# Optimization experiments

Hardware: AMD Instinct MI355X
Metric: run time of the kernel (lower is better)

Reference implementation:

```python
import jax, jax.numpy as jnp
import numpy as np

N = 100000   # nodes
E = 1600000  # edges (avg degree 16)
F_IN = 128   # num_features
H = 128      # num_hidden
C = 40       # num_classes


def setup_inputs() -> dict:
    key = jax.random.key(0)
    ks = jax.random.split(key, 8)
    w = lambda k, sh: jax.random.normal(k, sh, dtype=jnp.float32) * 0.05
    return {
        "x": jax.random.normal(ks[0], (N, F_IN), dtype=jnp.float32),
        "edge_index": jax.random.randint(ks[1], (2, E), 0, N),
        "W_rel1": w(ks[2], (F_IN, H)),
        "b_rel1": jnp.zeros((H,), jnp.float32),
        "W_root1": w(ks[3], (F_IN, H)),
        "W_rel2": w(ks[4], (H, H)),
        "b_rel2": jnp.zeros((H,), jnp.float32),
        "W_root2": w(ks[5], (H, H)),
        "W_lin": w(ks[6], (2 * H, C)),
        "b_lin": jnp.zeros((C,), jnp.float32),
    }


def _graph_conv(x, src, dst, W_rel, b_rel, W_root, n):
    # PyG GraphConv: sum_{j in N(i)} x_j -> lin_rel, plus lin_root(x_i)
    agg = jax.ops.segment_sum(x[src], dst, num_segments=n)  # [N, d_in]
    return agg @ W_rel + b_rel + x @ W_root


def reference(x, edge_index, W_rel1, b_rel1, W_root1, W_rel2, b_rel2, W_root2, W_lin, b_lin):
    src, dst = edge_index[0], edge_index[1]
    n = x.shape[0]
    # dropout is identity at inference (training=False)
    x1 = jax.nn.relu(_graph_conv(x, src, dst, W_rel1, b_rel1, W_root1, n))
    x2 = jax.nn.relu(_graph_conv(x1, src, dst, W_rel2, b_rel2, W_root2, n))
    h = jnp.concatenate([x1, x2], axis=-1)  # [N, 2H]
    return jax.nn.log_softmax(h @ W_lin + b_lin, axis=-1)
```

## Files before the change

### kernel.cpp

```cpp
#include <hip/hip_runtime.h>
#include <hip/hip_bf16.h>

typedef __attribute__((ext_vector_type(8))) short bf16x8;
typedef __attribute__((ext_vector_type(4))) float f32x4;

#define EPB 4096
#define BUCKET_BITS 10
#define BUCKET_SIZE 1024

static __device__ __forceinline__ unsigned short f2bf(float f) {
    union { float f; unsigned u; } v; v.f = f;
    unsigned r = v.u + 0x7FFF + ((v.u >> 16) & 1);
    return (unsigned short)(r >> 16);
}
static __device__ __forceinline__ float asf(unsigned u) {
    union { unsigned u; float f; } v; v.u = u;
    return v.f;
}

__global__ __launch_bounds__(256) void prep(const float* __restrict__ Wrel1,
                                            const float* __restrict__ Wroot1,
                                            const float* __restrict__ Wrel2,
                                            const float* __restrict__ Wroot2,
                                            const float* __restrict__ Wlin,
                                            const int* __restrict__ dst,
                                            unsigned short* __restrict__ bsw1,
                                            unsigned short* __restrict__ bsw2,
                                            unsigned short* __restrict__ bswL,
                                            int* __restrict__ hist,
                                            int E, int nblk, int nbuck) {
    __shared__ int h[128];
    int blk = blockIdx.x, t = threadIdx.x;
    if (blk < 256) {
        const float* Wrel  = (blk < 128) ? Wrel1 : Wrel2;
        const float* Wroot = (blk < 128) ? Wroot1 : Wroot2;
        unsigned short* bsw = (blk < 128) ? bsw1 : bsw2;
        int idx = (blk & 127) * 256 + t;
        int j = idx & 7, L = (idx >> 3) & 63, ct = (idx >> 9) & 15, kt = idx >> 13;
        int k = kt * 32 + ((L >> 4) * 8) + j;
        int c = ct * 16 + (L & 15);
        float v = (c < 128) ? Wrel[k * 128 + c] : Wroot[k * 128 + (c - 128)];
        bsw[idx] = f2bf(v);
    } else if (blk < 304) {
        int idx = (blk - 256) * 256 + t;
        int tt = idx;
        int j = tt & 7; tt >>= 3;
        int L = tt & 63; tt >>= 6;
        int ct = tt % 3;
        int kt = tt / 3;
        int k = kt * 32 + ((L >> 4) * 8) + j;
        int c = ct * 16 + (L & 15);
        float v = (c < 40) ? Wlin[k * 40 + c] : 0.f;
        bswL[idx] = f2bf(v);
    } else {
        int hb = blk - 304;
        if (t < nbuck) h[t] = 0;
        __syncthreads();
        int e0 = hb * EPB;
#pragma unroll
        for (int it = 0; it < EPB / 256; it++) {
            int e = e0 + it * 256 + t;
            if (e < E) atomicAdd(&h[dst[e] >> BUCKET_BITS], 1);
        }
        __syncthreads();
        if (t < nbuck) hist[t * nblk + hb] = h[t];
    }
}

__global__ __launch_bounds__(256) void scan_all(int* __restrict__ hist,
                                                int* __restrict__ bucketBase,
                                                int nblk, int nbuck) {
    __shared__ int tot[128];
    __shared__ int s[256];
    int b = blockIdx.x, t = threadIdx.x;
    if (t < 128) tot[t] = 0;
    __syncthreads();
    int len = nbuck * nblk;
    for (int i = t; i < len; i += 256) atomicAdd(&tot[i / nblk], hist[i]);
    __syncthreads();
    if (t < 128) s[t] = tot[t];
    __syncthreads();
#pragma unroll
    for (int o = 1; o < 128; o <<= 1) {
        int x = (t < 128 && t >= o) ? s[t - o] : 0;
        __syncthreads();
        if (t < 128) s[t] += x;
        __syncthreads();
    }
    int base_b = s[b] - tot[b];
    int tot_b = tot[b];
    if (t == 0) {
        bucketBase[b] = base_b;
        if (b == nbuck - 1) bucketBase[nbuck] = base_b + tot_b;
    }
    __syncthreads();
    int carryv = base_b;
    for (int start = 0; start < nblk; start += 256) {
        int i = start + t;
        int v = (i < nblk) ? hist[b * nblk + i] : 0;
        s[t] = v; __syncthreads();
#pragma unroll
        for (int o = 1; o < 256; o <<= 1) {
            int x = (t >= o) ? s[t - o] : 0;
            __syncthreads();
            s[t] += x; __syncthreads();
        }
        int excl = s[t] - v + carryv;
        if (i < nblk) hist[b * nblk + i] = excl;
        carryv += s[255];
        __syncthreads();
    }
}

__global__ __launch_bounds__(256) void edge_part(const int* __restrict__ src,
                                                 const int* __restrict__ dst,
                                                 const int* __restrict__ hist,
                                                 int* __restrict__ part,
                                                 int E, int nblk, int nbuck) {
    __shared__ int hcnt[128];
    __shared__ int lstart[128];
    __shared__ int cur[128];
    __shared__ int gbase[128];
    __shared__ int ssc[128];
    __shared__ int sdst[EPB];
    __shared__ int ssrc[EPB];
    int t = threadIdx.x, blk = blockIdx.x;
    int e0 = blk * EPB;
    int cnt = E - e0; if (cnt > EPB) cnt = EPB;
    if (t < nbuck) { hcnt[t] = 0; gbase[t] = hist[t * nblk + blk]; }
    __syncthreads();
    int myd[EPB / 256], mys[EPB / 256];
#pragma unroll
    for (int it = 0; it < EPB / 256; it++) {
        int i = it * 256 + t;
        if (i < cnt) {
            myd[it] = dst[e0 + i];
            mys[it] = src[e0 + i];
            atomicAdd(&hcnt[myd[it] >> BUCKET_BITS], 1);
        }
    }
    __syncthreads();
    if (t < 128) ssc[t] = (t < nbuck) ? hcnt[t] : 0;
    __syncthreads();
#pragma unroll
    for (int o = 1; o < 128; o <<= 1) {
        int x = 0;
        if (t < 128 && t >= o) x = ssc[t - o];
        __syncthreads();
        if (t < 128) ssc[t] += x;
        __syncthreads();
    }
    if (t < nbuck) { lstart[t] = ssc[t] - hcnt[t]; cur[t] = 0; }
    __syncthreads();
#pragma unroll
    for (int it = 0; it < EPB / 256; it++) {
        int i = it * 256 + t;
        if (i < cnt) {
            int b = myd[it] >> BUCKET_BITS;
            int p = lstart[b] + atomicAdd(&cur[b], 1);
            sdst[p] = myd[it];
            ssrc[p] = mys[it];
        }
    }
    __syncthreads();
    for (int i = t; i < cnt; i += 256) {
        int d = sdst[i], s = ssrc[i];
        int b = d >> BUCKET_BITS;
        part[gbase[b] + (i - lstart[b])] = ((d & (BUCKET_SIZE - 1)) << 17) | s;
    }
}

__global__ __launch_bounds__(256) void csrfin_gemm1(const int* __restrict__ part,
                                                    const int* __restrict__ bucketBase,
                                                    int* __restrict__ off_,
                                                    int* __restrict__ deg_,
                                                    int* __restrict__ csr_src,
                                                    const float* __restrict__ x,
                                                    const unsigned short* __restrict__ Bsw,
                                                    const float* __restrict__ bias,
                                                    unsigned short* __restrict__ xr,
                                                    unsigned short* __restrict__ accbf,
                                                    int N, int nbuck) {
    __shared__ int cur[BUCKET_SIZE];
    __shared__ int h[BUCKET_SIZE];
    __shared__ int tsum[256];
    int t = threadIdx.x;
    if (blockIdx.x < (unsigned)nbuck) {
        int b = blockIdx.x;
        int lo = bucketBase[b], hi = bucketBase[b + 1];
        int n0 = b * BUCKET_SIZE;
        for (int i = t; i < BUCKET_SIZE; i += 256) h[i] = 0;
        __syncthreads();
        for (int i = lo + t; i < hi; i += 256) atomicAdd(&h[part[i] >> 17], 1);
        __syncthreads();
        int a0 = h[4 * t], a1 = h[4 * t + 1], a2 = h[4 * t + 2], a3 = h[4 * t + 3];
        int ts = a0 + a1 + a2 + a3;
        tsum[t] = ts;
        __syncthreads();
#pragma unroll
        for (int o = 1; o < 256; o <<= 1) {
            int xx = (t >= o) ? tsum[t - o] : 0;
            __syncthreads();
            tsum[t] += xx;
            __syncthreads();
        }
        int st0 = tsum[t] - ts;
        int st1 = st0 + a0, st2 = st1 + a1, st3 = st2 + a2;
        cur[4 * t] = st0; cur[4 * t + 1] = st1; cur[4 * t + 2] = st2; cur[4 * t + 3] = st3;
        int node = n0 + 4 * t;
        if (node < N)     { off_[node] = lo + st0;     deg_[node] = a0; }
        if (node + 1 < N) { off_[node + 1] = lo + st1; deg_[node + 1] = a1; }
        if (node + 2 < N) { off_[node + 2] = lo + st2; deg_[node + 2] = a2; }
        if (node + 3 < N) { off_[node + 3] = lo + st3; deg_[node + 3] = a3; }
        __syncthreads();
        for (int i = lo + t; i < hi; i += 256) {
            int rec = part[i];
            int p = atomicAdd(&cur[rec >> 17], 1);
            csr_src[lo + p] = rec & 0x1FFFF;
        }
    } else {
        int wid = (blockIdx.x - nbuck) * 4 + (t >> 6);
        int L = t & 63;
        int r0 = wid * 16;
        if (r0 >= N) return;
        int arow = r0 + (L & 15);
        const bf16x8* Bptr = ((const bf16x8*)Bsw) + L;
        f32x4 acc[16];
#pragma unroll
        for (int i = 0; i < 16; i++) acc[i] = (f32x4){0.f, 0.f, 0.f, 0.f};
#pragma unroll
        for (int kt = 0; kt < 4; kt++) {
            const float* Arow = x + (size_t)arow * 128 + ((L >> 4) * 8) + kt * 32;
            float4 a0 = *(const float4*)Arow;
            float4 a1 = *(const float4*)(Arow + 4);
            bf16x8 a;
            a[0] = (short)f2bf(a0.x); a[1] = (short)f2bf(a0.y);
            a[2] = (short)f2bf(a0.z); a[3] = (short)f2bf(a0.w);
            a[4] = (short)f2bf(a1.x); a[5] = (short)f2bf(a1.y);
            a[6] = (short)f2bf(a1.z); a[7] = (short)f2bf(a1.w);
#pragma unroll
            for (int ct = 0; ct < 16; ct++) {
                bf16x8 b = Bptr[(kt * 16 + ct) * 64];
                acc[ct] = __builtin_amdgcn_mfma_f32_16x16x32_bf16(a, b, acc[ct], 0, 0, 0);
            }
        }
        int rbase = r0 + (L >> 4) * 4;
        int cl = L & 15;
#pragma unroll
        for (int ct = 0; ct < 16; ct++) {
            int col = ct * 16 + cl;
#pragma unroll
            for (int r = 0; r < 4; r++) {
                int row = rbase + r;
                float v = acc[ct][r];
                if (col < 128)
                    xr[(size_t)row * 128 + col] = f2bf(v);
                else
                    accbf[(size_t)row * 128 + (col - 128)] = f2bf(v + bias[col - 128]);
            }
        }
    }
}

__global__ __launch_bounds__(256) void gemm_layer2(const unsigned short* __restrict__ Abf,
                                                   const unsigned short* __restrict__ Bsw,
                                                   const float* __restrict__ bias,
                                                   unsigned short* __restrict__ xr,
                                                   unsigned short* __restrict__ accbf, int N) {
    int wid = blockIdx.x * 4 + (threadIdx.x >> 6);
    int L = threadIdx.x & 63;
    int r0 = wid * 16;
    if (r0 >= N) return;
    int arow = r0 + (L & 15);
    const bf16x8* Bptr = ((const bf16x8*)Bsw) + L;
    f32x4 acc[16];
#pragma unroll
    for (int i = 0; i < 16; i++) acc[i] = (f32x4){0.f, 0.f, 0.f, 0.f};
#pragma unroll
    for (int kt = 0; kt < 4; kt++) {
        bf16x8 a = *((const bf16x8*)(Abf + (size_t)arow * 128 + ((L >> 4) * 8) + kt * 32));
#pragma unroll
        for (int ct = 0; ct < 16; ct++) {
            bf16x8 b = Bptr[(kt * 16 + ct) * 64];
            acc[ct] = __builtin_amdgcn_mfma_f32_16x16x32_bf16(a, b, acc[ct], 0, 0, 0);
        }
    }
    int rbase = r0 + (L >> 4) * 4;
    int cl = L & 15;
#pragma unroll
    for (int ct = 0; ct < 16; ct++) {
        int col = ct * 16 + cl;
#pragma unroll
        for (int r = 0; r < 4; r++) {
            int row = rbase + r;
            float v = acc[ct][r];
            if (col < 128)
                xr[(size_t)row * 128 + col] = f2bf(v);
            else
                accbf[(size_t)row * 128 + (col - 128)] = f2bf(v + bias[col - 128]);
        }
    }
}

__global__ __launch_bounds__(256) void agg_relu_cvt(const unsigned short* __restrict__ xr,
                                                    const unsigned short* __restrict__ accbf,
                                                    const int* __restrict__ off_,
                                                    const int* __restrict__ deg,
                                                    const int* __restrict__ csr_src,
                                                    unsigned short* __restrict__ out, int N) {
    int node = blockIdx.x * 4 + (threadIdx.x >> 6);
    if (node >= N) return;
    int L = threadIdx.x & 63;
    int g = L >> 4;
    int f = L & 15;
    int o = off_[node];
    int d = deg[node];
    uint4 arow = (uint4){0, 0, 0, 0};
    if (g == 0) arow = *(const uint4*)(accbf + (size_t)node * 128 + f * 8);

    float lo0 = 0.f, lo1 = 0.f, lo2 = 0.f, lo3 = 0.f;
    float hi0 = 0.f, hi1 = 0.f, hi2 = 0.f, hi3 = 0.f;

    for (int k = 0; k < d; k += 64) {
        int chunk = (d - k < 64) ? (d - k) : 64;
        int id = (L < chunk) ? csr_src[o + k + L] : 0;
        int full = chunk & ~3;
#pragma unroll 4
        for (int j = 0; j < full; j += 4) {
            int s = __shfl(id, j + g, 64);
            uint4 p = *(const uint4*)(xr + (size_t)s * 128 + f * 8);
            lo0 += asf(p.x << 16); hi0 += asf(p.x & 0xFFFF0000u);
            lo1 += asf(p.y << 16); hi1 += asf(p.y & 0xFFFF0000u);
            lo2 += asf(p.z << 16); hi2 += asf(p.z & 0xFFFF0000u);
            lo3 += asf(p.w << 16); hi3 += asf(p.w & 0xFFFF0000u);
        }
        if (full < chunk) {
            int sl = full + g;
            int s = __shfl(id, (sl < chunk) ? sl : 0, 64);
            if (sl < chunk) {
                uint4 p = *(const uint4*)(xr + (size_t)s * 128 + f * 8);
                lo0 += asf(p.x << 16); hi0 += asf(p.x & 0xFFFF0000u);
                lo1 += asf(p.y << 16); hi1 += asf(p.y & 0xFFFF0000u);
                lo2 += asf(p.z << 16); hi2 += asf(p.z & 0xFFFF0000u);
                lo3 += asf(p.w << 16); hi3 += asf(p.w & 0xFFFF0000u);
            }
        }
    }
    lo0 += __shfl_xor(lo0, 16, 64); hi0 += __shfl_xor(hi0, 16, 64);
    lo1 += __shfl_xor(lo1, 16, 64); hi1 += __shfl_xor(hi1, 16, 64);
    lo2 += __shfl_xor(lo2, 16, 64); hi2 += __shfl_xor(hi2, 16, 64);
    lo3 += __shfl_xor(lo3, 16, 64); hi3 += __shfl_xor(hi3, 16, 64);
    lo0 += __shfl_xor(lo0, 32, 64); hi0 += __shfl_xor(hi0, 32, 64);
    lo1 += __shfl_xor(lo1, 32, 64); hi1 += __shfl_xor(hi1, 32, 64);
    lo2 += __shfl_xor(lo2, 32, 64); hi2 += __shfl_xor(hi2, 32, 64);
    lo3 += __shfl_xor(lo3, 32, 64); hi3 += __shfl_xor(hi3, 32, 64);

    if (g == 0) {
        uint4 wv;
        wv.x = ((unsigned)f2bf(fmaxf(asf(arow.x & 0xFFFF0000u) + hi0, 0.f)) << 16)
             | f2bf(fmaxf(asf(arow.x << 16) + lo0, 0.f));
        wv.y = ((unsigned)f2bf(fmaxf(asf(arow.y & 0xFFFF0000u) + hi1, 0.f)) << 16)
             | f2bf(fmaxf(asf(arow.y << 16) + lo1, 0.f));
        wv.z = ((unsigned)f2bf(fmaxf(asf(arow.z & 0xFFFF0000u) + hi2, 0.f)) << 16)
             | f2bf(fmaxf(asf(arow.z << 16) + lo2, 0.f));
        wv.w = ((unsigned)f2bf(fmaxf(asf(arow.w & 0xFFFF0000u) + hi3, 0.f)) << 16)
             | f2bf(fmaxf(asf(arow.w << 16) + lo3, 0.f));
        *(uint4*)(out + (size_t)node * 128 + f * 8) = wv;
    }
}

__global__ __launch_bounds__(256) void gemm_final_ls(const unsigned short* __restrict__ x1bf,
                                                     const unsigned short* __restrict__ x2bf,
                                                     const unsigned short* __restrict__ Bsw,
                                                     const float* __restrict__ blin,
                                                     float* __restrict__ out, int N) {
    int wid = blockIdx.x * 4 + (threadIdx.x >> 6);
    int L = threadIdx.x & 63;
    int r0 = wid * 16;
    if (r0 >= N) return;
    int arow = r0 + (L & 15);
    f32x4 acc[3];
#pragma unroll
    for (int i = 0; i < 3; i++) acc[i] = (f32x4){0.f, 0.f, 0.f, 0.f};
#pragma unroll
    for (int kt = 0; kt < 8; kt++) {
        const unsigned short* Ab = (kt < 4) ? x1bf : x2bf;
        int kk = (kt & 3) * 32 + ((L >> 4) * 8);
        bf16x8 a = *((const bf16x8*)(Ab + (size_t)arow * 128 + kk));
#pragma unroll
        for (int ct = 0; ct < 3; ct++) {
            bf16x8 b = ((const bf16x8*)Bsw)[(kt * 3 + ct) * 64 + L];
            acc[ct] = __builtin_amdgcn_mfma_f32_16x16x32_bf16(a, b, acc[ct], 0, 0, 0);
        }
    }
    int rbase = r0 + (L >> 4) * 4;
    int cl = L & 15;
    float b0 = blin[cl], b1 = blin[16 + cl];
    float b2 = (cl < 8) ? blin[32 + cl] : 0.f;
#pragma unroll
    for (int r = 0; r < 4; r++) {
        int row = rbase + r;
        float v0 = acc[0][r] + b0;
        float v1 = acc[1][r] + b1;
        float v2 = (cl < 8) ? (acc[2][r] + b2) : -__builtin_inff();
        float m = fmaxf(fmaxf(v0, v1), v2);
#pragma unroll
        for (int off = 8; off >= 1; off >>= 1) m = fmaxf(m, __shfl_xor(m, off, 64));
        float e = __expf(v0 - m) + __expf(v1 - m) + ((cl < 8) ? __expf(v2 - m) : 0.f);
#pragma unroll
        for (int off = 8; off >= 1; off >>= 1) e += __shfl_xor(e, off, 64);
        float ls = m + __logf(e);
        float* op = out + (size_t)row * 40;
        op[cl] = v0 - ls;
        op[16 + cl] = v1 - ls;
        if (cl < 8) op[32 + cl] = v2 - ls;
    }
}

extern "C" void kernel_launch(void* const* d_in, const int* in_sizes, int n_in,
                              void* d_out, int out_size, void* d_ws, size_t ws_size,
                              hipStream_t stream) {
    const float* x      = (const float*)d_in[0];
    const int*   edge   = (const int*)d_in[1];
    const float* Wrel1  = (const float*)d_in[2];
    const float* brel1  = (const float*)d_in[3];
    const float* Wroot1 = (const float*)d_in[4];
    const float* Wrel2  = (const float*)d_in[5];
    const float* brel2  = (const float*)d_in[6];
    const float* Wroot2 = (const float*)d_in[7];
    const float* Wlin   = (const float*)d_in[8];
    const float* blin   = (const float*)d_in[9];

    const int N = in_sizes[0] / 128;
    const int E = in_sizes[1] / 2;
    const int* src = edge;
    const int* dst = edge + E;

    const int nblk  = (E + EPB - 1) / EPB;
    const int nbuck = (N + BUCKET_SIZE - 1) / BUCKET_SIZE;

    char* ws = (char*)d_ws;
    size_t off = 0;
    auto alloc = [&](size_t bytes) -> void* {
        void* p = ws + off;
        off += (bytes + 255) & ~(size_t)255;
        return p;
    };
    unsigned short* x1bf = (unsigned short*)alloc((size_t)N * 128 * 2);
    unsigned short* x2bf = (unsigned short*)alloc((size_t)N * 128 * 2);
    unsigned short* xr   = (unsigned short*)alloc((size_t)N * 128 * 2);
    unsigned short* accbf= (unsigned short*)alloc((size_t)N * 128 * 2);
    unsigned short* bsw1 = (unsigned short*)alloc(32768 * 2);
    unsigned short* bsw2 = (unsigned short*)alloc(32768 * 2);
    unsigned short* bswL = (unsigned short*)alloc(12288 * 2);
    int* hist       = (int*)alloc((size_t)nbuck * nblk * 4);
    int* bucketBase = (int*)alloc((size_t)(nbuck + 1) * 4);
    int* part       = (int*)alloc((size_t)E * 4);
    int* csr_src    = (int*)alloc((size_t)E * 4);
    int* off_       = (int*)alloc((size_t)N * 4);
    int* deg_       = (int*)alloc((size_t)N * 4);

    const int rowTiles = (N + 15) / 16;
    const int gemmBlocks = (rowTiles + 3) / 4;
    const int nodeBlocks = (N + 3) / 4;

    prep<<<304 + nblk, 256, 0, stream>>>(Wrel1, Wroot1, Wrel2, Wroot2, Wlin, dst,
                                         bsw1, bsw2, bswL, hist, E, nblk, nbuck);
    scan_all<<<nbuck, 256, 0, stream>>>(hist, bucketBase, nblk, nbuck);
    edge_part<<<nblk, 256, 0, stream>>>(src, dst, hist, part, E, nblk, nbuck);
    csrfin_gemm1<<<nbuck + gemmBlocks, 256, 0, stream>>>(part, bucketBase, off_, deg_, csr_src,
                                                         x, bsw1, brel1, xr, accbf, N, nbuck);
    agg_relu_cvt<<<nodeBlocks, 256, 0, stream>>>(xr, accbf, off_, deg_, csr_src, x1bf, N);
    gemm_layer2<<<gemmBlocks, 256, 0, stream>>>(x1bf, bsw2, brel2, xr, accbf, N);
    agg_relu_cvt<<<nodeBlocks, 256, 0, stream>>>(xr, accbf, off_, deg_, csr_src, x2bf, N);
    gemm_final_ls<<<gemmBlocks, 256, 0, stream>>>(x1bf, x2bf, bswL, blin, (float*)d_out, N);
}
```

Measured before the change: 383.1 us.

## Use finer node buckets, split bucket scan into three kernels, simplify gather loop

Bucket size drops from 1024 to 256 nodes, so the number of buckets rises from about 98 to about 391. That gives the CSR-finalize phase four times as many blocks and one node per thread. The single scan_all kernel, which made every block redundantly atomically total the whole histogram, is replaced by three kernels: per-bucket totals, one scan over buckets, and a per-bucket block scan. The aggregation loop now has each lane read its neighbor index directly from csr_src instead of loading a 64-entry chunk and broadcasting it with shuffles. In exchange there are two more kernel launches, a larger histogram, and more shared-memory arrays in edge_part.

```diff
diff --git a/kernel.cpp b/kernel.cpp
--- a/kernel.cpp
+++ b/kernel.cpp
@@ -5,8 +5,9 @@
 typedef __attribute__((ext_vector_type(4))) float f32x4;
 
 #define EPB 4096
-#define BUCKET_BITS 10
-#define BUCKET_SIZE 1024
+#define BUCKET_BITS 8
+#define BUCKET_SIZE 256
+#define MAXBUCK 512
 
 static __device__ __forceinline__ unsigned short f2bf(float f) {
     union { float f; unsigned u; } v; v.f = f;
@@ -29,7 +30,7 @@
                                             unsigned short* __restrict__ bswL,
                                             int* __restrict__ hist,
                                             int E, int nblk, int nbuck) {
-    __shared__ int h[128];
+    __shared__ int h[MAXBUCK];
     int blk = blockIdx.x, t = threadIdx.x;
     if (blk < 256) {
         const float* Wrel  = (blk < 128) ? Wrel1 : Wrel2;
@@ -54,7 +55,7 @@
         bswL[idx] = f2bf(v);
     } else {
         int hb = blk - 304;
-        if (t < nbuck) h[t] = 0;
+        for (int i = t; i < MAXBUCK; i += 256) h[i] = 0;
         __syncthreads();
         int e0 = hb * EPB;
 #pragma unroll
@@ -63,38 +64,49 @@
             if (e < E) atomicAdd(&h[dst[e] >> BUCKET_BITS], 1);
         }
         __syncthreads();
-        if (t < nbuck) hist[t * nblk + hb] = h[t];
-    }
-}
-
-__global__ __launch_bounds__(256) void scan_all(int* __restrict__ hist,
-                                                int* __restrict__ bucketBase,
-                                                int nblk, int nbuck) {
-    __shared__ int tot[128];
+        for (int i = t; i < nbuck; i += 256) hist[i * nblk + hb] = h[i];
+    }
+}
+
+__global__ __launch_bounds__(256) void bucket_total(const int* __restrict__ hist,
+                                                    int* __restrict__ total, int nblk) {
     __shared__ int s[256];
     int b = blockIdx.x, t = threadIdx.x;
-    if (t < 128) tot[t] = 0;
-    __syncthreads();
-    int len = nbuck * nblk;
-    for (int i = t; i < len; i += 256) atomicAdd(&tot[i / nblk], hist[i]);
-    __syncthreads();
-    if (t < 128) s[t] = tot[t];
-    __syncthreads();
-#pragma unroll
-    for (int o = 1; o < 128; o <<= 1) {
-        int x = (t < 128 && t >= o) ? s[t - o] : 0;
-        __syncthreads();
-        if (t < 128) s[t] += x;
-        __syncthreads();
-    }
-    int base_b = s[b] - tot[b];
-    int tot_b = tot[b];
-    if (t == 0) {
-        bucketBase[b] = base_b;
-        if (b == nbuck - 1) bucketBase[nbuck] = base_b + tot_b;
-    }
-    __syncthreads();
-    int carryv = base_b;
+    int v = 0;
+    for (int i = t; i < nblk; i += 256) v += hist[b * nblk + i];
+    s[t] = v; __syncthreads();
+#pragma unroll
+    for (int o = 128; o >= 1; o >>= 1) {
+        if (t < o) s[t] += s[t + o];
+        __syncthreads();
+    }
+    if (t == 0) total[b] = s[0];
+}
+
+__global__ __launch_bounds__(256) void bucket_scan(const int* __restrict__ total,
+                                                   int* __restrict__ base, int nbuck) {
+    __shared__ int s[256];
+    int t = threadIdx.x;
+    int e0 = (2 * t < nbuck) ? total[2 * t] : 0;
+    int e1 = (2 * t + 1 < nbuck) ? total[2 * t + 1] : 0;
+    int ps = e0 + e1;
+    s[t] = ps; __syncthreads();
+#pragma unroll
+    for (int o = 1; o < 256; o <<= 1) {
+        int x = (t >= o) ? s[t - o] : 0;
+        __syncthreads();
+        s[t] += x; __syncthreads();
+    }
+    int pbase = s[t] - ps;
+    if (2 * t <= nbuck) base[2 * t] = pbase;
+    if (2 * t + 1 <= nbuck) base[2 * t + 1] = pbase + e0;
+}
+
+__global__ __launch_bounds__(256) void block_scan(int* __restrict__ hist,
+                                                  const int* __restrict__ base, int nblk) {
+    __shared__ int s[256];
+    int b = blockIdx.x, t = threadIdx.x;
+    int carryv = base[b];
     for (int start = 0; start < nblk; start += 256) {
         int i = start + t;
         int v = (i < nblk) ? hist[b * nblk + i] : 0;
@@ -117,17 +129,18 @@
                                                  const int* __restrict__ hist,
                                                  int* __restrict__ part,
                                                  int E, int nblk, int nbuck) {
-    __shared__ int hcnt[128];
-    __shared__ int lstart[128];
-    __shared__ int cur[128];
-    __shared__ int gbase[128];
-    __shared__ int ssc[128];
+    __shared__ int hcnt[MAXBUCK];
+    __shared__ int lstart[MAXBUCK];
+    __shared__ int cur[MAXBUCK];
+    __shared__ int gbase[MAXBUCK];
+    __shared__ int s2[256];
     __shared__ int sdst[EPB];
     __shared__ int ssrc[EPB];
     int t = threadIdx.x, blk = blockIdx.x;
     int e0 = blk * EPB;
     int cnt = E - e0; if (cnt > EPB) cnt = EPB;
-    if (t < nbuck) { hcnt[t] = 0; gbase[t] = hist[t * nblk + blk]; }
+    for (int i = t; i < MAXBUCK; i += 256) hcnt[i] = 0;
+    for (int i = t; i < nbuck; i += 256) gbase[i] = hist[i * nblk + blk];
     __syncthreads();
     int myd[EPB / 256], mys[EPB / 256];
 #pragma unroll
@@ -140,17 +153,18 @@
         }
     }
     __syncthreads();
-    if (t < 128) ssc[t] = (t < nbuck) ? hcnt[t] : 0;
-    __syncthreads();
-#pragma unroll
-    for (int o = 1; o < 128; o <<= 1) {
-        int x = 0;
-        if (t < 128 && t >= o) x = ssc[t - o];
-        __syncthreads();
-        if (t < 128) ssc[t] += x;
-        __syncthreads();
-    }
-    if (t < nbuck) { lstart[t] = ssc[t] - hcnt[t]; cur[t] = 0; }
+    int p0 = hcnt[2 * t], p1 = hcnt[2 * t + 1];
+    int ps = p0 + p1;
+    s2[t] = ps; __syncthreads();
+#pragma unroll
+    for (int o = 1; o < 256; o <<= 1) {
+        int x = (t >= o) ? s2[t - o] : 0;
+        __syncthreads();
+        s2[t] += x; __syncthreads();
+    }
+    int pbase = s2[t] - ps;
+    lstart[2 * t] = pbase; lstart[2 * t + 1] = pbase + p0;
+    cur[2 * t] = 0; cur[2 * t + 1] = 0;
     __syncthreads();
 #pragma unroll
     for (int it = 0; it < EPB / 256; it++) {
@@ -189,13 +203,12 @@
         int b = blockIdx.x;
         int lo = bucketBase[b], hi = bucketBase[b + 1];
         int n0 = b * BUCKET_SIZE;
-        for (int i = t; i < BUCKET_SIZE; i += 256) h[i] = 0;
+        h[t] = 0;
         __syncthreads();
         for (int i = lo + t; i < hi; i += 256) atomicAdd(&h[part[i] >> 17], 1);
         __syncthreads();
-        int a0 = h[4 * t], a1 = h[4 * t + 1], a2 = h[4 * t + 2], a3 = h[4 * t + 3];
-        int ts = a0 + a1 + a2 + a3;
-        tsum[t] = ts;
+        int hv = h[t];
+        tsum[t] = hv;
         __syncthreads();
 #pragma unroll
         for (int o = 1; o < 256; o <<= 1) {
@@ -204,14 +217,10 @@
             tsum[t] += xx;
             __syncthreads();
         }
-        int st0 = tsum[t] - ts;
-        int st1 = st0 + a0, st2 = st1 + a1, st3 = st2 + a2;
-        cur[4 * t] = st0; cur[4 * t + 1] = st1; cur[4 * t + 2] = st2; cur[4 * t + 3] = st3;
-        int node = n0 + 4 * t;
-        if (node < N)     { off_[node] = lo + st0;     deg_[node] = a0; }
-        if (node + 1 < N) { off_[node + 1] = lo + st1; deg_[node + 1] = a1; }
-        if (node + 2 < N) { off_[node + 2] = lo + st2; deg_[node + 2] = a2; }
-        if (node + 3 < N) { off_[node + 3] = lo + st3; deg_[node + 3] = a3; }
+        int st = tsum[t] - hv;
+        cur[t] = st;
+        int node = n0 + t;
+        if (node < N) { off_[node] = lo + st; deg_[node] = hv; }
         __syncthreads();
         for (int i = lo + t; i < hi; i += 256) {
             int rec = part[i];
@@ -318,33 +327,29 @@
     uint4 arow = (uint4){0, 0, 0, 0};
     if (g == 0) arow = *(const uint4*)(accbf + (size_t)node * 128 + f * 8);
 
+    const int* ip = csr_src + o + g;
+    const unsigned short* xrf = xr + f * 8;
+
     float lo0 = 0.f, lo1 = 0.f, lo2 = 0.f, lo3 = 0.f;
     float hi0 = 0.f, hi1 = 0.f, hi2 = 0.f, hi3 = 0.f;
 
-    for (int k = 0; k < d; k += 64) {
-        int chunk = (d - k < 64) ? (d - k) : 64;
-        int id = (L < chunk) ? csr_src[o + k + L] : 0;
-        int full = chunk & ~3;
+    int d4 = d & ~3;
 #pragma unroll 4
-        for (int j = 0; j < full; j += 4) {
-            int s = __shfl(id, j + g, 64);
-            uint4 p = *(const uint4*)(xr + (size_t)s * 128 + f * 8);
-            lo0 += asf(p.x << 16); hi0 += asf(p.x & 0xFFFF0000u);
-            lo1 += asf(p.y << 16); hi1 += asf(p.y & 0xFFFF0000u);
-            lo2 += asf(p.z << 16); hi2 += asf(p.z & 0xFFFF0000u);
-            lo3 += asf(p.w << 16); hi3 += asf(p.w & 0xFFFF0000u);
-        }
-        if (full < chunk) {
-            int sl = full + g;
-            int s = __shfl(id, (sl < chunk) ? sl : 0, 64);
-            if (sl < chunk) {
-                uint4 p = *(const uint4*)(xr + (size_t)s * 128 + f * 8);
-                lo0 += asf(p.x << 16); hi0 += asf(p.x & 0xFFFF0000u);
-                lo1 += asf(p.y << 16); hi1 += asf(p.y & 0xFFFF0000u);
-                lo2 += asf(p.z << 16); hi2 += asf(p.z & 0xFFFF0000u);
-                lo3 += asf(p.w << 16); hi3 += asf(p.w & 0xFFFF0000u);
-            }
-        }
+    for (int k = 0; k < d4; k += 4) {
+        int s = ip[k];
+        uint4 p = *(const uint4*)(xrf + (size_t)s * 128);
+        lo0 += asf(p.x << 16); hi0 += asf(p.x & 0xFFFF0000u);
+        lo1 += asf(p.y << 16); hi1 += asf(p.y & 0xFFFF0000u);
+        lo2 += asf(p.z << 16); hi2 += asf(p.z & 0xFFFF0000u);
+        lo3 += asf(p.w << 16); hi3 += asf(p.w & 0xFFFF0000u);
+    }
+    if (d4 + g < d) {
+        int s = ip[d4];
+        uint4 p = *(const uint4*)(xrf + (size_t)s * 128);
+        lo0 += asf(p.x << 16); hi0 += asf(p.x & 0xFFFF0000u);
+        lo1 += asf(p.y << 16); hi1 += asf(p.y & 0xFFFF0000u);
+        lo2 += asf(p.z << 16); hi2 += asf(p.z & 0xFFFF0000u);
+        lo3 += asf(p.w << 16); hi3 += asf(p.w & 0xFFFF0000u);
     }
     lo0 += __shfl_xor(lo0, 16, 64); hi0 += __shfl_xor(hi0, 16, 64);
     lo1 += __shfl_xor(lo1, 16, 64); hi1 += __shfl_xor(hi1, 16, 64);
@@ -454,6 +459,7 @@
     unsigned short* bsw2 = (unsigned short*)alloc(32768 * 2);
     unsigned short* bswL = (unsigned short*)alloc(12288 * 2);
     int* hist       = (int*)alloc((size_t)nbuck * nblk * 4);
+    int* bucketTot  = (int*)alloc((size_t)nbuck * 4);
     int* bucketBase = (int*)alloc((size_t)(nbuck + 1) * 4);
     int* part       = (int*)alloc((size_t)E * 4);
     int* csr_src    = (int*)alloc((size_t)E * 4);
@@ -466,7 +472,9 @@
 
     prep<<<304 + nblk, 256, 0, stream>>>(Wrel1, Wroot1, Wrel2, Wroot2, Wlin, dst,
                                          bsw1, bsw2, bswL, hist, E, nblk, nbuck);
-    scan_all<<<nbuck, 256, 0, stream>>>(hist, bucketBase, nblk, nbuck);
+    bucket_total<<<nbuck, 256, 0, stream>>>(hist, bucketTot, nblk);
+    bucket_scan<<<1, 256, 0, stream>>>(bucketTot, bucketBase, nbuck);
+    block_scan<<<nbuck, 256, 0, stream>>>(hist, bucketBase, nblk);
     edge_part<<<nblk, 256, 0, stream>>>(src, dst, hist, part, E, nblk, nbuck);
     csrfin_gemm1<<<nbuck + gemmBlocks, 256, 0, stream>>>(part, bucketBase, off_, deg_, csr_src,
                                                          x, bsw1, brel1, xr, accbf, N, nbuck);
```

After: 346.1 us. 1.11x faster.
